# Kernel optimization log

Hardware: AMD Instinct MI355X
Metric: run time of the kernel (lower is better)

The kernel has to match this reference:

```python
import jax, jax.numpy as jnp
import numpy as np

TIME_STEP = 7
B, C, D, H, W = 1, 3, 128, 160, 128


def grid_sample_3d(vol, grid):
    """Trilinear grid_sample, padding_mode='border', align_corners=True.
    vol: [B,C,D,H,W]; grid: [B,D,H,W,3] with last dim (x,y,z) in [-1,1]."""
    b, c, d, h, w = vol.shape
    # unnormalize (align_corners=True) and clamp to volume (border padding)
    ix = jnp.clip((grid[..., 0] + 1.0) * 0.5 * (w - 1), 0.0, w - 1)
    iy = jnp.clip((grid[..., 1] + 1.0) * 0.5 * (h - 1), 0.0, h - 1)
    iz = jnp.clip((grid[..., 2] + 1.0) * 0.5 * (d - 1), 0.0, d - 1)

    x0f = jnp.floor(ix); y0f = jnp.floor(iy); z0f = jnp.floor(iz)
    wx = (ix - x0f).reshape(b, 1, -1)
    wy = (iy - y0f).reshape(b, 1, -1)
    wz = (iz - z0f).reshape(b, 1, -1)

    x0 = x0f.astype(jnp.int32); x1 = jnp.minimum(x0 + 1, w - 1)
    y0 = y0f.astype(jnp.int32); y1 = jnp.minimum(y0 + 1, h - 1)
    z0 = z0f.astype(jnp.int32); z1 = jnp.minimum(z0 + 1, d - 1)

    vol_flat = vol.reshape(b, c, d * h * w)

    def gather(zi, yi, xi):
        idx = ((zi * h + yi) * w + xi).reshape(b, 1, -1)  # [B,1,N]
        return jnp.take_along_axis(vol_flat, idx, axis=2)  # [B,C,N]

    out = (gather(z0, y0, x0) * (1 - wz) * (1 - wy) * (1 - wx)
         + gather(z0, y0, x1) * (1 - wz) * (1 - wy) * wx
         + gather(z0, y1, x0) * (1 - wz) * wy * (1 - wx)
         + gather(z0, y1, x1) * (1 - wz) * wy * wx
         + gather(z1, y0, x0) * wz * (1 - wy) * (1 - wx)
         + gather(z1, y0, x1) * wz * (1 - wy) * wx
         + gather(z1, y1, x0) * wz * wy * (1 - wx)
         + gather(z1, y1, x1) * wz * wy * wx)
    return out.reshape(b, c, d, h, w)


def setup_inputs() -> dict:
    key = jax.random.key(0)
    k1, = jax.random.split(key, 1)
    velocity = jax.random.normal(k1, (B, C, D, H, W), dtype=jnp.float32)
    # identity sampling grid, normalized to [-1,1], last dim order (x,y,z)
    gz, gy, gx = jnp.meshgrid(
        jnp.linspace(-1.0, 1.0, D, dtype=jnp.float32),
        jnp.linspace(-1.0, 1.0, H, dtype=jnp.float32),
        jnp.linspace(-1.0, 1.0, W, dtype=jnp.float32),
        indexing='ij')
    sample_grid = jnp.broadcast_to(jnp.stack([gx, gy, gz], axis=-1)[None], (B, D, H, W, 3))
    range_flow = jnp.asarray(0.4, dtype=jnp.float32)
    return {"velocity": velocity, "sample_grid": sample_grid, "range_flow": range_flow}


def reference(velocity, sample_grid, range_flow):
    flow = velocity / (2.0 ** TIME_STEP)
    for _ in range(TIME_STEP):
        grid = sample_grid + jnp.transpose(flow, (0, 2, 3, 4, 1)) * range_flow
        flow = flow + grid_sample_3d(flow, grid)
    return flow
```

## Files before the change

### kernel.cpp

```cpp
#include <hip/hip_runtime.h>


constexpr int D = 128, H = 160, W = 128;
constexpr int N = D * H * W;
constexpr int VOX_BLOCKS = N / 256;
constexpr int NUM_XCD = 8;
constexpr int CHUNKS_PER_XCD = VOX_BLOCKS / NUM_XCD;

__global__ __launch_bounds__(256)
void repack_scale(const float* __restrict__ vel,
                  float3* __restrict__ dst3)
{
    const int i = blockIdx.x * blockDim.x + threadIdx.x;
    const float s = 1.0f / 128.0f;
    dst3[i] = make_float3(vel[i] * s, vel[i + N] * s, vel[i + 2 * N] * s);
}

template <bool PLANAR_OUT>
__global__ __launch_bounds__(256)
void diffeo_step(const float3* __restrict__ src3,
                 const float* __restrict__ rf_p,
                 void* __restrict__ dst_raw)
{
    const int b   = blockIdx.x;
    const int xcd = b & (NUM_XCD - 1);
    const int k   = b >> 3;
    const int vb  = xcd * CHUNKS_PER_XCD + k;
    const int i   = vb * 256 + threadIdx.x;

    const float rf = rf_p[0];

    const int x = i & (W - 1);
    const int r = i >> 7;
    const int y = r % H;
    const int z = r / H;

    const float3 f = src3[i];

    const float ix = fminf(fmaxf((float)x + f.x * (rf * 0.5f * (float)(W - 1)), 0.0f), (float)(W - 1));
    const float iy = fminf(fmaxf((float)y + f.y * (rf * 0.5f * (float)(H - 1)), 0.0f), (float)(H - 1));
    const float iz = fminf(fmaxf((float)z + f.z * (rf * 0.5f * (float)(D - 1)), 0.0f), (float)(D - 1));

    const float x0f = floorf(ix), y0f = floorf(iy), z0f = floorf(iz);
    const float wx = ix - x0f, wy = iy - y0f, wz = iz - z0f;
    const int x0 = (int)x0f, y0 = (int)y0f, z0 = (int)z0f;
    const int y1 = min(y0 + 1, H - 1);
    const int z1 = min(z0 + 1, D - 1);

    const int xb = min(x0, W - 2);
    const bool hix = (x0 == W - 1);

    int ofs[4];
    ofs[0] = (z0 * H + y0) * W + xb;
    ofs[1] = (z0 * H + y1) * W + xb;
    ofs[2] = (z1 * H + y0) * W + xb;
    ofs[3] = (z1 * H + y1) * W + xb;

    float3 p0[4], p1[4];
#pragma unroll
    for (int q = 0; q < 4; ++q) {
        p0[q] = src3[ofs[q]];
        p1[q] = src3[ofs[q] + 1];
    }
    if (hix) {
#pragma unroll
        for (int q = 0; q < 4; ++q) p0[q] = p1[q];
    }

    const float omx = 1.0f - wx, omy = 1.0f - wy, omz = 1.0f - wz;
    const float w00 = omz * omy, w01 = omz * wy, w10 = wz * omy, w11 = wz * wy;

    const float vx = w00 * (omx * p0[0].x + wx * p1[0].x)
                   + w01 * (omx * p0[1].x + wx * p1[1].x)
                   + w10 * (omx * p0[2].x + wx * p1[2].x)
                   + w11 * (omx * p0[3].x + wx * p1[3].x);
    const float vy = w00 * (omx * p0[0].y + wx * p1[0].y)
                   + w01 * (omx * p0[1].y + wx * p1[1].y)
                   + w10 * (omx * p0[2].y + wx * p1[2].y)
                   + w11 * (omx * p0[3].y + wx * p1[3].y);
    const float vz = w00 * (omx * p0[0].z + wx * p1[0].z)
                   + w01 * (omx * p0[1].z + wx * p1[1].z)
                   + w10 * (omx * p0[2].z + wx * p1[2].z)
                   + w11 * (omx * p0[3].z + wx * p1[3].z);

    const float o0 = f.x + vx, o1 = f.y + vy, o2 = f.z + vz;

    if (PLANAR_OUT) {
        float* __restrict__ dp = (float*)dst_raw;
        dp[i] = o0; dp[i + N] = o1; dp[i + 2 * N] = o2;
    } else {
        ((float3*)dst_raw)[i] = make_float3(o0, o1, o2);
    }
}

extern "C" void kernel_launch(void* const* d_in, const int* in_sizes, int n_in,
                              void* d_out, int out_size, void* d_ws, size_t ws_size,
                              hipStream_t stream)
{
    const float* vel = (const float*)d_in[0];
    const float* rf  = (const float*)d_in[2];
    float3* out3 = (float3*)d_out;
    float3* ws3  = (float3*)d_ws;

    const dim3 blk(256);
    const dim3 grd(VOX_BLOCKS);

    repack_scale<<<grd, blk, 0, stream>>>(vel, ws3);

    diffeo_step<false><<<grd, blk, 0, stream>>>(ws3,  rf, out3);
    diffeo_step<false><<<grd, blk, 0, stream>>>(out3, rf, ws3);
    diffeo_step<false><<<grd, blk, 0, stream>>>(ws3,  rf, out3);
    diffeo_step<false><<<grd, blk, 0, stream>>>(out3, rf, ws3);
    diffeo_step<false><<<grd, blk, 0, stream>>>(ws3,  rf, out3);
    diffeo_step<false><<<grd, blk, 0, stream>>>(out3, rf, ws3);
    diffeo_step<true ><<<grd, blk, 0, stream>>>(ws3,  rf, d_out);
}
```

Baseline: 297.1 us.

## Store intermediate flow in 2x2x2 cube-tiled float4 layout and fuse repack into first step

Intermediate flow fields are now stored as padded float4 entries arranged in 2x2x2 Morton-like cubes, and each block covers a 64x2x2 voxel brick, so the eight trilinear neighbours fall in nearby cache lines. The separate repack/scale kernel is gone; the first step reads the planar input directly and applies the 1/128 scale inline. Ping-pong buffers both live in workspace, at fixed offsets. The trade-off is that padding to float4 adds a third more memory traffic per voxel, in exchange for aligned single loads and better gather locality.

```diff
diff --git a/kernel.cpp b/kernel.cpp
--- a/kernel.cpp
+++ b/kernel.cpp
@@ -3,22 +3,21 @@
 
 constexpr int D = 128, H = 160, W = 128;
 constexpr int N = D * H * W;
-constexpr int VOX_BLOCKS = N / 256;
+constexpr int HC = H / 2, WC = W / 2;
+constexpr int NBLK = (D / 2) * (H / 2) * (W / 64);
 constexpr int NUM_XCD = 8;
-constexpr int CHUNKS_PER_XCD = VOX_BLOCKS / NUM_XCD;
+constexpr int CHUNKS_PER_XCD = NBLK / NUM_XCD;
 
-__global__ __launch_bounds__(256)
-void repack_scale(const float* __restrict__ vel,
-                  float3* __restrict__ dst3)
-{
-    const int i = blockIdx.x * blockDim.x + threadIdx.x;
-    const float s = 1.0f / 128.0f;
-    dst3[i] = make_float3(vel[i] * s, vel[i + N] * s, vel[i + 2 * N] * s);
+struct alignas(4) f2 { float a, b; };
+
+__device__ __forceinline__ int cube_idx(int z, int y, int x) {
+    return ((((z >> 1) * HC + (y >> 1)) * WC + (x >> 1)) << 3)
+         | ((z & 1) << 2) | ((y & 1) << 1) | (x & 1);
 }
 
-template <bool PLANAR_OUT>
+template <bool SRC_PLANAR, bool DST_PLANAR>
 __global__ __launch_bounds__(256)
-void diffeo_step(const float3* __restrict__ src3,
+void diffeo_step(const void* __restrict__ src_raw,
                  const float* __restrict__ rf_p,
                  void* __restrict__ dst_raw)
 {
@@ -26,16 +25,29 @@
     const int xcd = b & (NUM_XCD - 1);
     const int k   = b >> 3;
     const int vb  = xcd * CHUNKS_PER_XCD + k;
-    const int i   = vb * 256 + threadIdx.x;
+
+    const int zc  = vb / (HC * 2);
+    const int rem = vb - zc * (HC * 2);
+    const int yc  = rem >> 1;
+    const int xh  = rem & 1;
+
+    const int t = threadIdx.x;
+    const int x = (xh << 6) | (t & 63);
+    const int y = (yc << 1) | ((t >> 6) & 1);
+    const int z = (zc << 1) | (t >> 7);
 
     const float rf = rf_p[0];
+    const float s  = 1.0f / 128.0f;
 
-    const int x = i & (W - 1);
-    const int r = i >> 7;
-    const int y = r % H;
-    const int z = r / H;
-
-    const float3 f = src3[i];
+    float3 f;
+    if (SRC_PLANAR) {
+        const float* sp = (const float*)src_raw;
+        const int i = (z * H + y) * W + x;
+        f = make_float3(sp[i] * s, sp[i + N] * s, sp[i + 2 * N] * s);
+    } else {
+        const float4 v = ((const float4*)src_raw)[cube_idx(z, y, x)];
+        f = make_float3(v.x, v.y, v.z);
+    }
 
     const float ix = fminf(fmaxf((float)x + f.x * (rf * 0.5f * (float)(W - 1)), 0.0f), (float)(W - 1));
     const float iy = fminf(fmaxf((float)y + f.y * (rf * 0.5f * (float)(H - 1)), 0.0f), (float)(H - 1));
@@ -47,24 +59,41 @@
     const int y1 = min(y0 + 1, H - 1);
     const int z1 = min(z0 + 1, D - 1);
 
-    const int xb = min(x0, W - 2);
-    const bool hix = (x0 == W - 1);
+    float3 p0[4], p1[4];
 
-    int ofs[4];
-    ofs[0] = (z0 * H + y0) * W + xb;
-    ofs[1] = (z0 * H + y1) * W + xb;
-    ofs[2] = (z1 * H + y0) * W + xb;
-    ofs[3] = (z1 * H + y1) * W + xb;
-
-    float3 p0[4], p1[4];
+    if (SRC_PLANAR) {
+        const float* sp = (const float*)src_raw;
+        const int xb = min(x0, W - 2);
+        const bool hix = (x0 == W - 1);
+        int ofs[4];
+        ofs[0] = (z0 * H + y0) * W + xb;
+        ofs[1] = (z0 * H + y1) * W + xb;
+        ofs[2] = (z1 * H + y0) * W + xb;
+        ofs[3] = (z1 * H + y1) * W + xb;
 #pragma unroll
-    for (int q = 0; q < 4; ++q) {
-        p0[q] = src3[ofs[q]];
-        p1[q] = src3[ofs[q] + 1];
-    }
-    if (hix) {
+        for (int q = 0; q < 4; ++q) {
+            const f2 px = *(const f2*)(sp + ofs[q]);
+            const f2 py = *(const f2*)(sp + N + ofs[q]);
+            const f2 pz = *(const f2*)(sp + 2 * N + ofs[q]);
+            p0[q] = make_float3(px.a * s, py.a * s, pz.a * s);
+            p1[q] = make_float3(px.b * s, py.b * s, pz.b * s);
+        }
+        if (hix) {
 #pragma unroll
-        for (int q = 0; q < 4; ++q) p0[q] = p1[q];
+            for (int q = 0; q < 4; ++q) p0[q] = p1[q];
+        }
+    } else {
+        const float4* sc = (const float4*)src_raw;
+        const int x1 = min(x0 + 1, W - 1);
+#pragma unroll
+        for (int q = 0; q < 4; ++q) {
+            const int zi = (q & 2) ? z1 : z0;
+            const int yi = (q & 1) ? y1 : y0;
+            const float4 a  = sc[cube_idx(zi, yi, x0)];
+            const float4 bq = sc[cube_idx(zi, yi, x1)];
+            p0[q] = make_float3(a.x, a.y, a.z);
+            p1[q] = make_float3(bq.x, bq.y, bq.z);
+        }
     }
 
     const float omx = 1.0f - wx, omy = 1.0f - wy, omz = 1.0f - wz;
@@ -85,11 +114,12 @@
 
     const float o0 = f.x + vx, o1 = f.y + vy, o2 = f.z + vz;
 
-    if (PLANAR_OUT) {
+    if (DST_PLANAR) {
         float* __restrict__ dp = (float*)dst_raw;
+        const int i = (z * H + y) * W + x;
         dp[i] = o0; dp[i + N] = o1; dp[i + 2 * N] = o2;
     } else {
-        ((float3*)dst_raw)[i] = make_float3(o0, o1, o2);
+        ((float4*)dst_raw)[cube_idx(z, y, x)] = make_float4(o0, o1, o2, 0.0f);
     }
 }
 
@@ -99,19 +129,18 @@
 {
     const float* vel = (const float*)d_in[0];
     const float* rf  = (const float*)d_in[2];
-    float3* out3 = (float3*)d_out;
-    float3* ws3  = (float3*)d_ws;
+
+    float4* A = (float4*)d_ws;
+    float4* B = (float4*)((char*)d_ws + (size_t)48 * 1024 * 1024);
 
     const dim3 blk(256);
-    const dim3 grd(VOX_BLOCKS);
+    const dim3 grd(NBLK);
 
-    repack_scale<<<grd, blk, 0, stream>>>(vel, ws3);
-
-    diffeo_step<false><<<grd, blk, 0, stream>>>(ws3,  rf, out3);
-    diffeo_step<false><<<grd, blk, 0, stream>>>(out3, rf, ws3);
-    diffeo_step<false><<<grd, blk, 0, stream>>>(ws3,  rf, out3);
-    diffeo_step<false><<<grd, blk, 0, stream>>>(out3, rf, ws3);
-    diffeo_step<false><<<grd, blk, 0, stream>>>(ws3,  rf, out3);
-    diffeo_step<false><<<grd, blk, 0, stream>>>(out3, rf, ws3);
-    diffeo_step<true ><<<grd, blk, 0, stream>>>(ws3,  rf, d_out);
+    diffeo_step<true , false><<<grd, blk, 0, stream>>>(vel, rf, A);
+    diffeo_step<false, false><<<grd, blk, 0, stream>>>(A,   rf, B);
+    diffeo_step<false, false><<<grd, blk, 0, stream>>>(B,   rf, A);
+    diffeo_step<false, false><<<grd, blk, 0, stream>>>(A,   rf, B);
+    diffeo_step<false, false><<<grd, blk, 0, stream>>>(B,   rf, A);
+    diffeo_step<false, false><<<grd, blk, 0, stream>>>(A,   rf, B);
+    diffeo_step<false, true ><<<grd, blk, 0, stream>>>(B,   rf, d_out);
 }
```

Measured after the change: 360.2 us. 1.21x slower.
